# Optimization experiments

Measured on AMD Instinct MI355X. Metric: run time of the kernel, lower is better.

## Reference

```python
import jax, jax.numpy as jnp
import numpy as np

E = 1024   # embed_dim
H = 16     # num_heads
D = E // H # head_dim = 64
B = 2
S = 2048

def setup_inputs() -> dict:
    key = jax.random.key(0)
    ks = jax.random.split(key, 11)
    std = 0.02
    return {
        "query": jax.random.normal(ks[0], (B, S, E), jnp.float32),
        "key":   jax.random.normal(ks[1], (B, S, E), jnp.float32),
        "value": jax.random.normal(ks[2], (B, S, E), jnp.float32),
        "Wq": std * jax.random.normal(ks[3], (E, E), jnp.float32),
        "bq": jnp.zeros((E,), jnp.float32),
        "Wk": std * jax.random.normal(ks[4], (D, E), jnp.float32),
        "bk": jnp.zeros((D,), jnp.float32),
        "Wv": std * jax.random.normal(ks[5], (D, E), jnp.float32),
        "bv": jnp.zeros((D,), jnp.float32),
        "Wo": std * jax.random.normal(ks[6], (E, E), jnp.float32),
        "bo": jnp.zeros((E,), jnp.float32),
    }

def reference(query, key, value, Wq, bq, Wk, bk, Wv, bv, Wo, bo):
    b, t, _ = query.shape
    scaling = D ** -0.5
    q = query @ Wq.T + bq                      # [B, T, E]
    k = key @ Wk.T + bk                        # [B, S, D] (single shared KV head)
    v = value @ Wv.T + bv                      # [B, S, D]
    q = q.reshape(b, t, H, D).transpose(0, 2, 1, 3) * scaling  # [B, H, T, D]
    # MQA: broadcast shared k/v across heads inside einsum (no materialized expand)
    attn_weights = jnp.einsum("bhtd,bsd->bhts", q, k)          # [B, H, T, S]
    attn_probs = jax.nn.softmax(attn_weights, axis=-1)
    attn_output = jnp.einsum("bhts,bsd->bhtd", attn_probs, v)  # [B, H, T, D]
    attn_output = attn_output.transpose(0, 2, 1, 3).reshape(b, t, E)
    return attn_output @ Wo.T + bo
```

## Files before the change

### kernel.cpp

```cpp
#include <hip/hip_runtime.h>

#define E_DIM  1024
#define H_HEADS 16
#define D_HEAD  64
#define B_BATCH 2
#define S_SEQ  2048
#define M_ROWS (B_BATCH * S_SEQ)

typedef unsigned short u16;
typedef unsigned int   u32;
typedef __attribute__((ext_vector_type(8))) short bf16x8;
typedef __attribute__((ext_vector_type(4))) short bf16x4;
typedef __attribute__((ext_vector_type(4))) float f32x4;

#define MFMA32(a, b, c) __builtin_amdgcn_mfma_f32_16x16x32_bf16(a, b, c, 0, 0, 0)

#if __has_builtin(__builtin_amdgcn_mfma_f32_16x16x16bf16_1k)
#define HAVE_MFMA16 1
#define MFMA16(a, b, c) __builtin_amdgcn_mfma_f32_16x16x16bf16_1k(a, b, c, 0, 0, 0)
#else
#define HAVE_MFMA16 0
#endif

__device__ __forceinline__ u16 f2bf(float f) {
    union { float f; u32 i; } x; x.f = f;
    u32 r = x.i + 0x7fffu + ((x.i >> 16) & 1u);
    return (u16)(r >> 16);
}

#if __has_builtin(__builtin_amdgcn_cvt_pk_bf16_f32)
typedef __attribute__((ext_vector_type(2))) __bf16 bfp2;
__device__ __forceinline__ u32 pk2(float a, float b) {
    bfp2 t = __builtin_amdgcn_cvt_pk_bf16_f32(a, b);
    union { bfp2 v; u32 u; } c; c.v = t; return c.u;
}
#else
__device__ __forceinline__ u32 pk2(float a, float b) {
    return (u32)f2bf(a) | ((u32)f2bf(b) << 16);
}
#endif

__device__ __forceinline__ bf16x8 cvt8(const float4& a, const float4& b) {
    union { u32 u[4]; bf16x8 v; } t;
    t.u[0] = pk2(a.x, a.y); t.u[1] = pk2(a.z, a.w);
    t.u[2] = pk2(b.x, b.y); t.u[3] = pk2(b.z, b.w);
    return t.v;
}
__device__ __forceinline__ bf16x4 pack4(const f32x4& v) {
    union { u32 u[2]; bf16x4 w; } t;
    t.u[0] = pk2(v[0], v[1]); t.u[1] = pk2(v[2], v[3]);
    return t.w;
}

__device__ __forceinline__ void gl_lds16(const u16* g, u16* l) {
    __builtin_amdgcn_global_load_lds(
        (const __attribute__((address_space(1))) u32*)g,
        (__attribute__((address_space(3))) u32*)l, 16, 0, 0);
}

__global__ __launch_bounds__(256) void cast_w_kernel(
    const float* __restrict__ W, u16* __restrict__ out)
{
    const size_t i = (size_t)(blockIdx.x * 256 + threadIdx.x) * 8;
    float4 a = ((const float4*)(W + i))[0];
    float4 b = ((const float4*)(W + i))[1];
    *(bf16x8*)(out + i) = cvt8(a, b);
}

template<typename TA, bool OUT_BF16>
__global__ __launch_bounds__(512, 2) void gemm128_kernel(
    const TA* __restrict__ A, const u16* __restrict__ W,
    const float* __restrict__ bias, void* __restrict__ Cv,
    int M, int N, int K, float scale)
{
    __shared__ u16 Asm[2][2][128 * 32];
    __shared__ u16 Bsm[2][2][128 * 32];

    const int tid = threadIdx.x;
    const int w  = tid >> 6;
    const int ln = tid & 63;
    const int n  = ln & 15;
    const int qd = ln >> 4;
    const int wm = (w & 1) * 64;
    const int wn = (w >> 1) * 32;

    const int m0 = blockIdx.y * 128;
    const int n0 = blockIdx.x * 128;

    const int srow = tid >> 2;
    const int sblk = tid & 3;
    const int sc   = (sblk ^ (srow & 3)) * 8;

    f32x4 acc[4][2];
#pragma unroll
    for (int mt = 0; mt < 4; mt++)
#pragma unroll
        for (int nt = 0; nt < 2; nt++) acc[mt][nt] = (f32x4){0.f, 0.f, 0.f, 0.f};

    float4 areg[2][2];

    auto stageA16 = [&](int p, int k0) {
#pragma unroll
        for (int kb = 0; kb < 2; kb++)
            gl_lds16((const u16*)A + (size_t)(m0 + srow) * K + k0 + kb * 32 + sc,
                     &Asm[p][kb][srow * 32 + sblk * 8]);
    };
    auto stageB16 = [&](int p, int k0) {
#pragma unroll
        for (int kb = 0; kb < 2; kb++)
            gl_lds16(W + (size_t)(n0 + srow) * K + k0 + kb * 32 + sc,
                     &Bsm[p][kb][srow * 32 + sblk * 8]);
    };
    auto loadA_f32 = [&](int k0) {
#pragma unroll
        for (int kb = 0; kb < 2; kb++) {
            const float* pa = (const float*)A + (size_t)(m0 + srow) * K + k0 + kb * 32 + sc;
            areg[kb][0] = ((const float4*)pa)[0];
            areg[kb][1] = ((const float4*)pa)[1];
        }
    };
    auto writeA_f32 = [&](int p) {
#pragma unroll
        for (int kb = 0; kb < 2; kb++)
            *(bf16x8*)&Asm[p][kb][srow * 32 + sblk * 8] = cvt8(areg[kb][0], areg[kb][1]);
    };
    auto compute = [&](int p) {
        bf16x8 af[4][2], bfr[2][2];
#pragma unroll
        for (int kb = 0; kb < 2; kb++) {
#pragma unroll
            for (int mt = 0; mt < 4; mt++) {
                int r = wm + mt * 16 + n;
                af[mt][kb] = *(const bf16x8*)&Asm[p][kb][r * 32 + ((qd ^ (n & 3)) * 8)];
            }
#pragma unroll
            for (int nt = 0; nt < 2; nt++) {
                int r = wn + nt * 16 + n;
                bfr[nt][kb] = *(const bf16x8*)&Bsm[p][kb][r * 32 + ((qd ^ (n & 3)) * 8)];
            }
        }
#pragma unroll
        for (int kb = 0; kb < 2; kb++)
#pragma unroll
            for (int mt = 0; mt < 4; mt++)
#pragma unroll
                for (int nt = 0; nt < 2; nt++)
                    acc[mt][nt] = MFMA32(af[mt][kb], bfr[nt][kb], acc[mt][nt]);
    };

    if constexpr (sizeof(TA) == 4) { loadA_f32(0); writeA_f32(0); }
    else                           { stageA16(0, 0); }
    stageB16(0, 0);

    int p = 0;
    for (int k0 = 64; k0 < K; k0 += 64) {
        __syncthreads();
        if constexpr (sizeof(TA) == 4) {
            loadA_f32(k0);
            stageB16(p ^ 1, k0);
            compute(p);
            writeA_f32(p ^ 1);
        } else {
            stageA16(p ^ 1, k0);
            stageB16(p ^ 1, k0);
            compute(p);
        }
        p ^= 1;
    }
    __syncthreads();
    compute(p);

    float bb[2];
#pragma unroll
    for (int nt = 0; nt < 2; nt++) bb[nt] = bias[n0 + wn + nt * 16 + n] * scale;

#pragma unroll
    for (int mt = 0; mt < 4; mt++)
#pragma unroll
        for (int r = 0; r < 4; r++) {
            const int row = m0 + wm + mt * 16 + qd * 4 + r;
#pragma unroll
            for (int nt = 0; nt < 2; nt++) {
                const int col = n0 + wn + nt * 16 + n;
                float v = acc[mt][nt][r] * scale + bb[nt];
                if (OUT_BF16) ((u16*)Cv)[(size_t)row * N + col] = f2bf(v);
                else        ((float*)Cv)[(size_t)row * N + col] = v;
            }
        }
}

__global__ __launch_bounds__(256) void kv_proj_kernel(
    const float* __restrict__ key, const float* __restrict__ value,
    const float* __restrict__ Wk, const float* __restrict__ Wv,
    const float* __restrict__ bk, const float* __restrict__ bv,
    u16* __restrict__ Kout, u16* __restrict__ VTout, int M, int K)
{
    const bool vproj = (blockIdx.y == 1);
    const float* A    = vproj ? value : key;
    const float* W    = vproj ? Wv : Wk;
    const float* bias = vproj ? bv : bk;

    __shared__ u16 Asm[64 * 32];
    __shared__ u16 Bsm[64 * 32];

    const int tid = threadIdx.x;
    const int w  = tid >> 6;
    const int ln = tid & 63;
    const int n  = ln & 15;
    const int qd = ln >> 4;
    const int wm = (w & 1) * 32;
    const int wn = (w >> 1) * 32;
    const int m0 = blockIdx.x * 64;

    const int srow = tid >> 2;
    const int scol = (tid & 3) * 8;

    f32x4 acc[2][2];
#pragma unroll
    for (int mt = 0; mt < 2; mt++)
#pragma unroll
        for (int nt = 0; nt < 2; nt++) acc[mt][nt] = (f32x4){0.f, 0.f, 0.f, 0.f};

    for (int k0 = 0; k0 < K; k0 += 32) {
        __syncthreads();
        const float* pa = A + (size_t)(m0 + srow) * K + k0 + scol;
        const float* pw = W + (size_t)srow * K + k0 + scol;
        float4 a0 = ((const float4*)pa)[0], a1 = ((const float4*)pa)[1];
        float4 w0 = ((const float4*)pw)[0], w1 = ((const float4*)pw)[1];
        *(bf16x8*)&Asm[srow * 32 + scol] = cvt8(a0, a1);
        *(bf16x8*)&Bsm[srow * 32 + scol] = cvt8(w0, w1);
        __syncthreads();

        bf16x8 af[2], bfr[2];
#pragma unroll
        for (int t = 0; t < 2; t++) {
            af[t]  = *(const bf16x8*)&Asm[(wm + t * 16 + n) * 32 + qd * 8];
            bfr[t] = *(const bf16x8*)&Bsm[(wn + t * 16 + n) * 32 + qd * 8];
        }
#pragma unroll
        for (int mt = 0; mt < 2; mt++)
#pragma unroll
            for (int nt = 0; nt < 2; nt++)
                acc[mt][nt] = MFMA32(af[mt], bfr[nt], acc[mt][nt]);
    }

    if (!vproj) {
#pragma unroll
        for (int mt = 0; mt < 2; mt++)
#pragma unroll
            for (int r = 0; r < 4; r++) {
                const int row = m0 + wm + mt * 16 + qd * 4 + r;
#pragma unroll
                for (int nt = 0; nt < 2; nt++) {
                    const int col = wn + nt * 16 + n;
                    Kout[(size_t)row * 64 + col] = f2bf(acc[mt][nt][r] + bias[col]);
                }
            }
    } else {
#pragma unroll
        for (int mt = 0; mt < 2; mt++)
#pragma unroll
            for (int nt = 0; nt < 2; nt++) {
                const int col = wn + nt * 16 + n;
                const int row0 = m0 + wm + mt * 16 + qd * 4;
                float b4 = bias[col];
                ushort4 pk;
                pk.x = f2bf(acc[mt][nt][0] + b4);
                pk.y = f2bf(acc[mt][nt][1] + b4);
                pk.z = f2bf(acc[mt][nt][2] + b4);
                pk.w = f2bf(acc[mt][nt][3] + b4);
                *(ushort4*)&VTout[(size_t)col * M + row0] = pk;
            }
    }
}

__global__ __launch_bounds__(256, 3) void mqa_attn_mfma_kernel(
    const u16* Q, const u16* __restrict__ K,
    const u16* __restrict__ VT, u16* O)
{
    __shared__ u16 ksm[2][128 * 32];
    __shared__ u16 vsm[4][64 * 32];
#if !HAVE_MFMA16
    __shared__ u16 psm[4][32 * 128];
#endif

    const int tid = threadIdx.x;
    const int w   = tid >> 6;
    const int ln  = tid & 63;
    const int n   = ln & 15;
    const int qd  = ln >> 4;
    const int lr  = ln >> 2;
    const int blk = ln & 3;
    const int rb  = lr & 3;

    const int bid = blockIdx.x;
    const int qb = bid & 15;
    const int h  = (bid >> 4) & (H_HEADS - 1);
    const int b  = bid >> 8;
    const int q0 = qb * 128;

    {
        const u16* qg = Q + (size_t)(b * S_SEQ + q0) * E_DIM + h * 64;
#pragma unroll
        for (int kb = 0; kb < 2; kb++)
#pragma unroll
            for (int j = 0; j < 2; j++) {
                int row = w * 32 + j * 16 + lr;
                gl_lds16(qg + (size_t)row * E_DIM + kb * 32 + ((blk ^ rb) * 8),
                         &ksm[kb][row * 32 + blk * 8]);
            }
    }
    __syncthreads();

    bf16x8 qa[2][2];
#pragma unroll
    for (int mt = 0; mt < 2; mt++)
#pragma unroll
        for (int kb = 0; kb < 2; kb++) {
            int row = w * 32 + mt * 16 + n;
            qa[mt][kb] = *(const bf16x8*)&ksm[kb][row * 32 + ((qd ^ (n & 3)) * 8)];
        }

    f32x4 acc_o[2][4];
    float lsum[2] = {0.f, 0.f};
#pragma unroll
    for (int mt = 0; mt < 2; mt++)
#pragma unroll
        for (int ntd = 0; ntd < 4; ntd++) acc_o[mt][ntd] = (f32x4){0.f, 0.f, 0.f, 0.f};

    const u16* kg = K  + (size_t)b * S_SEQ * 64;
    const u16* vg = VT + (size_t)b * S_SEQ;

    for (int s0 = 0; s0 < S_SEQ; s0 += 128) {
        __syncthreads();
#pragma unroll
        for (int kb = 0; kb < 2; kb++)
#pragma unroll
            for (int j = 0; j < 2; j++) {
                int row = w * 32 + j * 16 + lr;
                gl_lds16(kg + (size_t)(s0 + row) * 64 + kb * 32 + ((blk ^ rb) * 8),
                         &ksm[kb][row * 32 + blk * 8]);
            }
#pragma unroll
        for (int j = 0; j < 4; j++) {
            int d = j * 16 + lr;
            gl_lds16(vg + (size_t)d * M_ROWS + s0 + w * 32 + ((blk ^ rb) * 8),
                     &vsm[w][d * 32 + blk * 8]);
        }
        __syncthreads();

        f32x4 sacc[2][8];
#pragma unroll
        for (int mt = 0; mt < 2; mt++)
#pragma unroll
            for (int nt = 0; nt < 8; nt++) sacc[mt][nt] = (f32x4){0.f, 0.f, 0.f, 0.f};
#pragma unroll
        for (int nt = 0; nt < 8; nt++) {
            int rowk = nt * 16 + n;
#pragma unroll
            for (int kb = 0; kb < 2; kb++) {
                bf16x8 kf = *(const bf16x8*)&ksm[kb][rowk * 32 + ((qd ^ (n & 3)) * 8)];
                sacc[0][nt] = MFMA32(kf, qa[0][kb], sacc[0][nt]);
                sacc[1][nt] = MFMA32(kf, qa[1][kb], sacc[1][nt]);
            }
        }

        bf16x4 pa[2][8];
#pragma unroll
        for (int mt = 0; mt < 2; mt++) {
            float ls = 0.f;
#pragma unroll
            for (int nt = 0; nt < 8; nt++) {
#pragma unroll
                for (int r = 0; r < 4; r++) {
                    float pv = exp2f(sacc[mt][nt][r]);
                    sacc[mt][nt][r] = pv;
                    ls += pv;
                }
                pa[mt][nt] = pack4(sacc[mt][nt]);
            }
            lsum[mt] += ls;
        }

#if HAVE_MFMA16
#pragma unroll
        for (int kk = 0; kk < 8; kk++) {
            int c = kk >> 1;
            int lblk = (kk & 1) * 2 + (qd >> 1);
#pragma unroll
            for (int ntd = 0; ntd < 4; ntd++) {
                int d = ntd * 16 + n;
                bf16x4 bv = *(const bf16x4*)
                    &vsm[c][d * 32 + ((lblk ^ (n & 3)) * 8) + (qd & 1) * 4];
                acc_o[0][ntd] = MFMA16(pa[0][kk], bv, acc_o[0][ntd]);
                acc_o[1][ntd] = MFMA16(pa[1][kk], bv, acc_o[1][ntd]);
            }
        }
#else
#pragma unroll
        for (int mt = 0; mt < 2; mt++)
#pragma unroll
            for (int nt = 0; nt < 8; nt++) {
                int t = mt * 16 + n;
                int lb = nt * 2 + (qd >> 1);
                union { bf16x4 v; uint2 u; } pw; pw.v = pa[mt][nt];
                *(uint2*)&psm[w][t * 128 + ((lb ^ n) * 8) + (qd & 1) * 4] = pw.u;
            }
#pragma unroll
        for (int kb = 0; kb < 4; kb++) {
            bf16x8 paf[2];
#pragma unroll
            for (int mt = 0; mt < 2; mt++) {
                int t = mt * 16 + n;
                paf[mt] = *(const bf16x8*)&psm[w][t * 128 + (((kb * 4 + qd) ^ n) * 8)];
            }
#pragma unroll
            for (int ntd = 0; ntd < 4; ntd++) {
                int d = ntd * 16 + n;
                bf16x8 bv = *(const bf16x8*)&vsm[kb][d * 32 + ((qd ^ (n & 3)) * 8)];
                acc_o[0][ntd] = MFMA32(paf[0], bv, acc_o[0][ntd]);
                acc_o[1][ntd] = MFMA32(paf[1], bv, acc_o[1][ntd]);
            }
        }
#endif
    }

#pragma unroll
    for (int mt = 0; mt < 2; mt++) {
        lsum[mt] += __shfl_xor(lsum[mt], 16);
        lsum[mt] += __shfl_xor(lsum[mt], 32);
    }
#pragma unroll
    for (int mt = 0; mt < 2; mt++)
#pragma unroll
        for (int r = 0; r < 4; r++) {
            float inv = 1.f / __shfl(lsum[mt], qd * 4 + r);
            int grow = b * S_SEQ + q0 + w * 32 + mt * 16 + qd * 4 + r;
#pragma unroll
            for (int ntd = 0; ntd < 4; ntd++) {
                int gcol = h * D_HEAD + ntd * 16 + n;
                O[(size_t)grow * E_DIM + gcol] = f2bf(acc_o[mt][ntd][r] * inv);
            }
        }
}

extern "C" void kernel_launch(void* const* d_in, const int* in_sizes, int n_in,
                              void* d_out, int out_size, void* d_ws, size_t ws_size,
                              hipStream_t stream) {
    const float* query = (const float*)d_in[0];
    const float* key   = (const float*)d_in[1];
    const float* value = (const float*)d_in[2];
    const float* Wq    = (const float*)d_in[3];
    const float* bq    = (const float*)d_in[4];
    const float* Wk    = (const float*)d_in[5];
    const float* bk    = (const float*)d_in[6];
    const float* Wv    = (const float*)d_in[7];
    const float* bv    = (const float*)d_in[8];
    const float* Wo    = (const float*)d_in[9];
    const float* bo    = (const float*)d_in[10];
    float* out = (float*)d_out;

    const int M = M_ROWS;

    u16* q_bf  = (u16*)d_ws;
    u16* k_bf  = q_bf + (size_t)M * E_DIM;
    u16* vt_bf = k_bf + (size_t)M * D_HEAD;
    u16* w_bf  = vt_bf + (size_t)M * D_HEAD;

    dim3 blk(256);
    const float scaling = 0.125f * 1.44269504088896f;

    cast_w_kernel<<<dim3(E_DIM * E_DIM / 2048), blk, 0, stream>>>(Wq, w_bf);

    kv_proj_kernel<<<dim3(M / 64, 2), blk, 0, stream>>>(
        key, value, Wk, Wv, bk, bv, k_bf, vt_bf, M, E_DIM);

    gemm128_kernel<float, true><<<dim3(E_DIM / 128, M / 128), dim3(512), 0, stream>>>(
        query, w_bf, bq, q_bf, M, E_DIM, E_DIM, scaling);

    cast_w_kernel<<<dim3(E_DIM * E_DIM / 2048), blk, 0, stream>>>(Wo, w_bf);

    mqa_attn_mfma_kernel<<<dim3(B_BATCH * H_HEADS * (S_SEQ / 128)), blk, 0, stream>>>(
        q_bf, k_bf, vt_bf, q_bf);

    gemm128_kernel<u16, false><<<dim3(E_DIM / 128, M / 128), dim3(512), 0, stream>>>(
        q_bf, w_bf, bo, out, M, E_DIM, E_DIM, 1.0f);
}
```

Before: 258.1 us.

## Pre-cast query to bf16, merge casts, and use 128x64 tiles in 256-thread GEMM

A single combined kernel now converts the query activations, Wq and Wo to bf16 in one launch, replacing two separate weight casts. The query bf16 copy is written into the output buffer as scratch. The projection GEMM changes from 512-thread 128x128 tiles to 256-thread 128x64 tiles with a bf16-only async LDS path, doubling the grid and dropping the in-loop fp32 conversion. The cost is an extra full pass over the query tensor in memory and reuse of the output buffer as temporary storage.

```diff
diff --git a/kernel.cpp b/kernel.cpp
--- a/kernel.cpp
+++ b/kernel.cpp
@@ -58,23 +58,30 @@
         (__attribute__((address_space(3))) u32*)l, 16, 0, 0);
 }
 
-__global__ __launch_bounds__(256) void cast_w_kernel(
-    const float* __restrict__ W, u16* __restrict__ out)
+__global__ __launch_bounds__(256) void cast_all_kernel(
+    const float* __restrict__ q,  const float* __restrict__ wq,
+    const float* __restrict__ wo,
+    u16* __restrict__ qo, u16* __restrict__ wqo, u16* __restrict__ woo)
 {
-    const size_t i = (size_t)(blockIdx.x * 256 + threadIdx.x) * 8;
-    float4 a = ((const float4*)(W + i))[0];
-    float4 b = ((const float4*)(W + i))[1];
-    *(bf16x8*)(out + i) = cvt8(a, b);
-}
-
-template<typename TA, bool OUT_BF16>
-__global__ __launch_bounds__(512, 2) void gemm128_kernel(
-    const TA* __restrict__ A, const u16* __restrict__ W,
+    const int bid = blockIdx.x;
+    const float* src; u16* dst; size_t base;
+    if (bid < 2048)      { src = q;  dst = qo;  base = (size_t)bid * 2048; }
+    else if (bid < 2560) { src = wq; dst = wqo; base = (size_t)(bid - 2048) * 2048; }
+    else                 { src = wo; dst = woo; base = (size_t)(bid - 2560) * 2048; }
+    const size_t i = base + (size_t)threadIdx.x * 8;
+    float4 a = ((const float4*)(src + i))[0];
+    float4 b = ((const float4*)(src + i))[1];
+    *(bf16x8*)(dst + i) = cvt8(a, b);
+}
+
+template<bool OUT_BF16>
+__global__ __launch_bounds__(256, 2) void gemm_bf16_kernel(
+    const u16* __restrict__ A, const u16* __restrict__ W,
     const float* __restrict__ bias, void* __restrict__ Cv,
     int M, int N, int K, float scale)
 {
     __shared__ u16 Asm[2][2][128 * 32];
-    __shared__ u16 Bsm[2][2][128 * 32];
+    __shared__ u16 Bsm[2][2][64 * 32];
 
     const int tid = threadIdx.x;
     const int w  = tid >> 6;
@@ -85,7 +92,7 @@
     const int wn = (w >> 1) * 32;
 
     const int m0 = blockIdx.y * 128;
-    const int n0 = blockIdx.x * 128;
+    const int n0 = blockIdx.x * 64;
 
     const int srow = tid >> 2;
     const int sblk = tid & 3;
@@ -97,45 +104,34 @@
 #pragma unroll
         for (int nt = 0; nt < 2; nt++) acc[mt][nt] = (f32x4){0.f, 0.f, 0.f, 0.f};
 
-    float4 areg[2][2];
-
-    auto stageA16 = [&](int p, int k0) {
+    auto stageA = [&](int p, int k0) {
 #pragma unroll
         for (int kb = 0; kb < 2; kb++)
-            gl_lds16((const u16*)A + (size_t)(m0 + srow) * K + k0 + kb * 32 + sc,
-                     &Asm[p][kb][srow * 32 + sblk * 8]);
+#pragma unroll
+            for (int g = 0; g < 2; g++) {
+                const int row = g * 64 + srow;
+                gl_lds16(A + (size_t)(m0 + row) * K + k0 + kb * 32 + sc,
+                         &Asm[p][kb][row * 32 + sblk * 8]);
+            }
     };
-    auto stageB16 = [&](int p, int k0) {
+    auto stageB = [&](int p, int k0) {
 #pragma unroll
         for (int kb = 0; kb < 2; kb++)
             gl_lds16(W + (size_t)(n0 + srow) * K + k0 + kb * 32 + sc,
                      &Bsm[p][kb][srow * 32 + sblk * 8]);
     };
-    auto loadA_f32 = [&](int k0) {
-#pragma unroll
-        for (int kb = 0; kb < 2; kb++) {
-            const float* pa = (const float*)A + (size_t)(m0 + srow) * K + k0 + kb * 32 + sc;
-            areg[kb][0] = ((const float4*)pa)[0];
-            areg[kb][1] = ((const float4*)pa)[1];
-        }
-    };
-    auto writeA_f32 = [&](int p) {
-#pragma unroll
-        for (int kb = 0; kb < 2; kb++)
-            *(bf16x8*)&Asm[p][kb][srow * 32 + sblk * 8] = cvt8(areg[kb][0], areg[kb][1]);
-    };
     auto compute = [&](int p) {
         bf16x8 af[4][2], bfr[2][2];
 #pragma unroll
         for (int kb = 0; kb < 2; kb++) {
 #pragma unroll
             for (int mt = 0; mt < 4; mt++) {
-                int r = wm + mt * 16 + n;
+                const int r = wm + mt * 16 + n;
                 af[mt][kb] = *(const bf16x8*)&Asm[p][kb][r * 32 + ((qd ^ (n & 3)) * 8)];
             }
 #pragma unroll
             for (int nt = 0; nt < 2; nt++) {
-                int r = wn + nt * 16 + n;
+                const int r = wn + nt * 16 + n;
                 bfr[nt][kb] = *(const bf16x8*)&Bsm[p][kb][r * 32 + ((qd ^ (n & 3)) * 8)];
             }
         }
@@ -148,23 +144,14 @@
                     acc[mt][nt] = MFMA32(af[mt][kb], bfr[nt][kb], acc[mt][nt]);
     };
 
-    if constexpr (sizeof(TA) == 4) { loadA_f32(0); writeA_f32(0); }
-    else                           { stageA16(0, 0); }
-    stageB16(0, 0);
+    stageA(0, 0); stageB(0, 0);
 
     int p = 0;
     for (int k0 = 64; k0 < K; k0 += 64) {
         __syncthreads();
-        if constexpr (sizeof(TA) == 4) {
-            loadA_f32(k0);
-            stageB16(p ^ 1, k0);
-            compute(p);
-            writeA_f32(p ^ 1);
-        } else {
-            stageA16(p ^ 1, k0);
-            stageB16(p ^ 1, k0);
-            compute(p);
-        }
+        stageA(p ^ 1, k0);
+        stageB(p ^ 1, k0);
+        compute(p);
         p ^= 1;
     }
     __syncthreads();
@@ -465,24 +452,26 @@
     u16* q_bf  = (u16*)d_ws;
     u16* k_bf  = q_bf + (size_t)M * E_DIM;
     u16* vt_bf = k_bf + (size_t)M * D_HEAD;
-    u16* w_bf  = vt_bf + (size_t)M * D_HEAD;
+    u16* wq_bf = vt_bf + (size_t)M * D_HEAD;
+    u16* wo_bf = wq_bf + (size_t)E_DIM * E_DIM;
+
+    u16* qc_bf = (u16*)d_out;
 
     dim3 blk(256);
     const float scaling = 0.125f * 1.44269504088896f;
 
-    cast_w_kernel<<<dim3(E_DIM * E_DIM / 2048), blk, 0, stream>>>(Wq, w_bf);
+    cast_all_kernel<<<dim3(3072), blk, 0, stream>>>(
+        query, Wq, Wo, qc_bf, wq_bf, wo_bf);
 
     kv_proj_kernel<<<dim3(M / 64, 2), blk, 0, stream>>>(
         key, value, Wk, Wv, bk, bv, k_bf, vt_bf, M, E_DIM);
 
-    gemm128_kernel<float, true><<<dim3(E_DIM / 128, M / 128), dim3(512), 0, stream>>>(
-        query, w_bf, bq, q_bf, M, E_DIM, E_DIM, scaling);
-
-    cast_w_kernel<<<dim3(E_DIM * E_DIM / 2048), blk, 0, stream>>>(Wo, w_bf);
+    gemm_bf16_kernel<true><<<dim3(E_DIM / 64, M / 128), blk, 0, stream>>>(
+        qc_bf, wq_bf, bq, q_bf, M, E_DIM, E_DIM, scaling);
 
     mqa_attn_mfma_kernel<<<dim3(B_BATCH * H_HEADS * (S_SEQ / 128)), blk, 0, stream>>>(
         q_bf, k_bf, vt_bf, q_bf);
 
-    gemm128_kernel<u16, false><<<dim3(E_DIM / 128, M / 128), dim3(512), 0, stream>>>(
-        q_bf, w_bf, bo, out, M, E_DIM, E_DIM, 1.0f);
-}
+    gemm_bf16_kernel<false><<<dim3(E_DIM / 64, M / 128), blk, 0, stream>>>(
+        q_bf, wo_bf, bo, out, M, E_DIM, E_DIM, 1.0f);
+}
```

After: 260.6 us. No clear change (+1.0%).
